# Kernel optimization log

Measured on AMD Instinct MI355X. Metric: run time of the kernel, lower is better.

## Reference

```python
import jax, jax.numpy as jnp
import numpy as np

NUM_CLUSTERS = 64
DIM = 512
ALPHA = 100.0
EPS = 1e-12  # torch F.normalize eps


def setup_inputs() -> dict:
    key = jax.random.key(0)
    k1, k2 = jax.random.split(key)
    x1 = jax.random.normal(k1, (30, DIM, 28, 28), dtype=jnp.float32)
    centroids = jax.random.uniform(k2, (NUM_CLUSTERS, DIM), dtype=jnp.float32)
    # _init_params: conv weight = 2*alpha*centroids (1x1 conv), bias = -alpha*||centroid||
    conv_w = 2.0 * ALPHA * centroids
    conv_b = -ALPHA * jnp.linalg.norm(centroids, axis=1)
    return {"x1": x1, "centroids": centroids, "conv_w": conv_w, "conv_b": conv_b}


def _l2norm(v, axis):
    n = jnp.sqrt(jnp.sum(v * v, axis=axis, keepdims=True))
    return v / jnp.maximum(n, EPS)


def reference(x1, centroids, conv_w, conv_b):
    T, C, H, W = x1.shape
    K, D = centroids.shape
    x = x1.reshape(T, C, H * W)            # [T, C, N]
    x = _l2norm(x, axis=1)                 # normalize_input: L2 over channel dim
    # 1x1 conv == matmul over channels: logits [T, K, N]
    logits = jnp.einsum('kc,tcn->tkn', conv_w, x) + conv_b[None, :, None]
    a = jax.nn.softmax(logits, axis=1)     # soft assignment over clusters
    # vlad[t,k,c] = sum_n a[t,k,n]*(x[t,c,n] - centroids[k,c])
    # rewritten as two small matmuls, avoiding the [K,C,N] residual tensor
    vlad = jnp.einsum('tkn,tcn->tkc', a, x) - a.sum(axis=-1)[:, :, None] * centroids[None]
    vlad = _l2norm(vlad, axis=2)           # intra-normalization over feature dim
    v = vlad.reshape(T, K * D)
    v = _l2norm(v, axis=1)                 # global L2 normalization
    return v.sum(axis=0, keepdims=True)    # [1, K*D] accumulated over 30 timesteps
```

## Files before the change

kernel.cpp:

```cpp
#include <hip/hip_runtime.h>
#include <math.h>

#define T_ 30
#define C_ 512
#define N_ 784
#define NA_ 800
#define XPITCH 520
#define EPSV 1e-12f

typedef __attribute__((ext_vector_type(8))) short bf16x8;
typedef __attribute__((ext_vector_type(4))) float f32x4;

__device__ __forceinline__ unsigned short f2bf(float f) {
    union { float f; unsigned int u; } v; v.f = f;
    unsigned int r = (v.u + 0x7FFFu + ((v.u >> 16) & 1u)) >> 16;
    return (unsigned short)r;
}
__device__ __forceinline__ float bf2f(unsigned short h) {
    union { unsigned int u; float f; } v; v.u = ((unsigned int)h) << 16;
    return v.f;
}

__global__ void k_prep(const float* __restrict__ w, unsigned short* __restrict__ wh,
                       unsigned short* __restrict__ wl) {
    int idx = blockIdx.x * 256 + threadIdx.x;
    float v = w[idx];
    unsigned short h = f2bf(v);
    wh[idx] = h;
    wl[idx] = f2bf(v - bf2f(h));
}

__global__ __launch_bounds__(256, 4) void k_assign(
    const float* __restrict__ x, const unsigned short* __restrict__ wh,
    const unsigned short* __restrict__ wl, const float* __restrict__ b,
    unsigned short* __restrict__ aT, float* __restrict__ asum)
{
    __shared__ __align__(16) char smem[2 * 16 * XPITCH * 2];
    unsigned short* xh = (unsigned short*)smem;
    unsigned short* xl = xh + 16 * XPITCH;
    float* red = (float*)smem;
    __shared__ float ssq[4][16];

    int t = blockIdx.y, n0 = blockIdx.x * 16;
    int tid = threadIdx.x;
    int w = tid >> 6, L = tid & 63, lid = L & 15, quad = L >> 4;
    int cbase = w * 128;
    int nseg = (L & 3) * 4;
    int crow = L >> 2;

    float4 q[8];
    #pragma unroll
    for (int p = 0; p < 8; ++p) {
        int c = cbase + p * 16 + crow;
        q[p] = *reinterpret_cast<const float4*>(
            x + ((size_t)t * C_ + c) * N_ + n0 + nseg);
    }
    float bk = b[L];

    const unsigned short* wha = wh + (size_t)lid * C_ + cbase + quad * 8;
    const unsigned short* wla = wl + (size_t)lid * C_ + cbase + quad * 8;
    bf16x8 cah[4], cal[4];
    #pragma unroll
    for (int mt = 0; mt < 4; ++mt) {
        cah[mt] = *reinterpret_cast<const bf16x8*>(wha + mt * 16 * C_);
        cal[mt] = *reinterpret_cast<const bf16x8*>(wla + mt * 16 * C_);
    }

    float ss0 = 0.f, ss1 = 0.f, ss2 = 0.f, ss3 = 0.f;
    #pragma unroll
    for (int p = 0; p < 8; ++p) {
        int c = cbase + p * 16 + crow;
        float vv[4] = {q[p].x, q[p].y, q[p].z, q[p].w};
        ss0 = fmaf(vv[0], vv[0], ss0); ss1 = fmaf(vv[1], vv[1], ss1);
        ss2 = fmaf(vv[2], vv[2], ss2); ss3 = fmaf(vv[3], vv[3], ss3);
        #pragma unroll
        for (int j = 0; j < 4; ++j) {
            unsigned short h = f2bf(vv[j]);
            xh[(nseg + j) * XPITCH + c] = h;
            xl[(nseg + j) * XPITCH + c] = f2bf(vv[j] - bf2f(h));
        }
    }
    #pragma unroll
    for (int m = 4; m <= 32; m <<= 1) {
        ss0 += __shfl_xor(ss0, m, 64); ss1 += __shfl_xor(ss1, m, 64);
        ss2 += __shfl_xor(ss2, m, 64); ss3 += __shfl_xor(ss3, m, 64);
    }
    if (L < 4) {
        ssq[w][L * 4 + 0] = ss0; ssq[w][L * 4 + 1] = ss1;
        ssq[w][L * 4 + 2] = ss2; ssq[w][L * 4 + 3] = ss3;
    }

    f32x4 acc[4];
    #pragma unroll
    for (int mt = 0; mt < 4; ++mt)
        #pragma unroll
        for (int r = 0; r < 4; ++r) acc[mt][r] = 0.f;

    #pragma unroll
    for (int ks = 0; ks < 4; ++ks) {
        bf16x8 nah[4], nal[4];
        #pragma unroll
        for (int mt = 0; mt < 4; ++mt) { nah[mt] = cah[mt]; nal[mt] = cal[mt]; }
        if (ks < 3) {
            #pragma unroll
            for (int mt = 0; mt < 4; ++mt) {
                nah[mt] = *reinterpret_cast<const bf16x8*>(
                    wha + mt * 16 * C_ + (ks + 1) * 32);
                nal[mt] = *reinterpret_cast<const bf16x8*>(
                    wla + mt * 16 * C_ + (ks + 1) * 32);
            }
        }
        int cs = cbase + ks * 32;
        bf16x8 bh = *reinterpret_cast<const bf16x8*>(&xh[lid * XPITCH + cs + quad * 8]);
        bf16x8 bl = *reinterpret_cast<const bf16x8*>(&xl[lid * XPITCH + cs + quad * 8]);
        #pragma unroll
        for (int mt = 0; mt < 4; ++mt) {
            acc[mt] = __builtin_amdgcn_mfma_f32_16x16x32_bf16(cah[mt], bh, acc[mt], 0, 0, 0);
            acc[mt] = __builtin_amdgcn_mfma_f32_16x16x32_bf16(cal[mt], bh, acc[mt], 0, 0, 0);
            acc[mt] = __builtin_amdgcn_mfma_f32_16x16x32_bf16(cah[mt], bl, acc[mt], 0, 0, 0);
        }
        #pragma unroll
        for (int mt = 0; mt < 4; ++mt) { cah[mt] = nah[mt]; cal[mt] = nal[mt]; }
    }
    __syncthreads();
    {
        float* rp = red + w * (16 * 68);
        #pragma unroll
        for (int mt = 0; mt < 4; ++mt)
            *reinterpret_cast<f32x4*>(&rp[lid * 68 + mt * 16 + quad * 4]) = acc[mt];
    }
    __syncthreads();

    float vv[4], iv[4];
    #pragma unroll
    for (int i = 0; i < 4; ++i) {
        int n = w * 4 + i;
        float s = ssq[0][n] + ssq[1][n] + ssq[2][n] + ssq[3][n];
        iv[i] = 1.0f / fmaxf(sqrtf(s), EPSV);
        float v = red[0 * 1088 + n * 68 + L] + red[1 * 1088 + n * 68 + L]
                + red[2 * 1088 + n * 68 + L] + red[3 * 1088 + n * 68 + L];
        vv[i] = fmaf(v, iv[i], bk);
    }
    float mx[4] = {vv[0], vv[1], vv[2], vv[3]};
    #pragma unroll
    for (int m = 1; m <= 32; m <<= 1) {
        #pragma unroll
        for (int i = 0; i < 4; ++i) mx[i] = fmaxf(mx[i], __shfl_xor(mx[i], m, 64));
    }
    float e[4], se[4];
    #pragma unroll
    for (int i = 0; i < 4; ++i) { e[i] = __expf(vv[i] - mx[i]); se[i] = e[i]; }
    #pragma unroll
    for (int m = 1; m <= 32; m <<= 1) {
        #pragma unroll
        for (int i = 0; i < 4; ++i) se[i] += __shfl_xor(se[i], m, 64);
    }
    float asl = 0.f;
    unsigned short av[4];
    #pragma unroll
    for (int i = 0; i < 4; ++i) {
        float a = e[i] / se[i];
        av[i] = f2bf(a * iv[i]);
        asl += a;
    }
    atomicAdd(&asum[t * 64 + L], asl);
    ushort4 st; st.x = av[0]; st.y = av[1]; st.z = av[2]; st.w = av[3];
    *reinterpret_cast<ushort4*>(aT + ((size_t)t * 64 + L) * NA_ + n0 + w * 4) = st;
    if (blockIdx.x == 48) {
        ushort4 z; z.x = 0; z.y = 0; z.z = 0; z.w = 0;
        *reinterpret_cast<ushort4*>(aT + ((size_t)t * 64 + L) * NA_ + 784 + w * 4) = z;
    }
}

__global__ __launch_bounds__(256) void k_vlad(
    const float* __restrict__ x, const unsigned short* __restrict__ aT,
    const float* __restrict__ asum, const float* __restrict__ cent,
    float* __restrict__ vlad, float* __restrict__ g2)
{
    __shared__ float red[4][16 * 68];
    int t = blockIdx.y, c0 = blockIdx.x * 16;
    int tid = threadIdx.x;
    int w = tid >> 6, L = tid & 63, lid = L & 15, quad = L >> 4;

    f32x4 acc[4];
    #pragma unroll
    for (int mt = 0; mt < 4; ++mt)
        #pragma unroll
        for (int r = 0; r < 4; ++r) acc[mt][r] = 0.f;

    const float* xrow = x + ((size_t)t * C_ + c0 + lid) * N_;
    const unsigned short* a0 = aT + (size_t)t * 64 * NA_ + (size_t)lid * NA_;

    int k = tid >> 2, cs4 = (tid & 3) * 4;
    float as = asum[t * 64 + k];
    float4 cv = *reinterpret_cast<const float4*>(cent + k * C_ + c0 + cs4);

    int nb = w * 32 + quad * 8;
    int nc = nb > 776 ? 776 : nb;
    float4 x0c = *reinterpret_cast<const float4*>(xrow + nc);
    float4 x1c = *reinterpret_cast<const float4*>(xrow + nc + 4);
    bf16x8 f0 = *reinterpret_cast<const bf16x8*>(a0 + nb);
    bf16x8 f1 = *reinterpret_cast<const bf16x8*>(a0 + 16 * NA_ + nb);
    bf16x8 f2 = *reinterpret_cast<const bf16x8*>(a0 + 32 * NA_ + nb);
    bf16x8 f3 = *reinterpret_cast<const bf16x8*>(a0 + 48 * NA_ + nb);

    for (int s = w; s < 25; s += 4) {
        int sn = s + 4;
        float4 x0n = x0c, x1n = x1c;
        bf16x8 g0 = f0, g1 = f1, g2v = f2, g3 = f3;
        if (sn < 25) {
            int nb2 = sn * 32 + quad * 8;
            int nc2 = nb2 > 776 ? 776 : nb2;
            x0n = *reinterpret_cast<const float4*>(xrow + nc2);
            x1n = *reinterpret_cast<const float4*>(xrow + nc2 + 4);
            g0 = *reinterpret_cast<const bf16x8*>(a0 + nb2);
            g1 = *reinterpret_cast<const bf16x8*>(a0 + 16 * NA_ + nb2);
            g2v = *reinterpret_cast<const bf16x8*>(a0 + 32 * NA_ + nb2);
            g3 = *reinterpret_cast<const bf16x8*>(a0 + 48 * NA_ + nb2);
        }
        bf16x8 bb;
        bb[0] = (short)f2bf(x0c.x); bb[1] = (short)f2bf(x0c.y);
        bb[2] = (short)f2bf(x0c.z); bb[3] = (short)f2bf(x0c.w);
        bb[4] = (short)f2bf(x1c.x); bb[5] = (short)f2bf(x1c.y);
        bb[6] = (short)f2bf(x1c.z); bb[7] = (short)f2bf(x1c.w);
        acc[0] = __builtin_amdgcn_mfma_f32_16x16x32_bf16(f0, bb, acc[0], 0, 0, 0);
        acc[1] = __builtin_amdgcn_mfma_f32_16x16x32_bf16(f1, bb, acc[1], 0, 0, 0);
        acc[2] = __builtin_amdgcn_mfma_f32_16x16x32_bf16(f2, bb, acc[2], 0, 0, 0);
        acc[3] = __builtin_amdgcn_mfma_f32_16x16x32_bf16(f3, bb, acc[3], 0, 0, 0);
        x0c = x0n; x1c = x1n; f0 = g0; f1 = g1; f2 = g2v; f3 = g3;
    }
    {
        float* rp = &red[w][0];
        #pragma unroll
        for (int mt = 0; mt < 4; ++mt)
            *reinterpret_cast<f32x4*>(&rp[lid * 68 + mt * 16 + quad * 4]) = acc[mt];
    }
    __syncthreads();

    float4 vout;
    float s2 = 0.f;
    #pragma unroll
    for (int j = 0; j < 4; ++j) {
        int cc = cs4 + j;
        float v = red[0][cc * 68 + k] + red[1][cc * 68 + k]
                + red[2][cc * 68 + k] + red[3][cc * 68 + k];
        v -= as * ((const float*)&cv)[j];
        ((float*)&vout)[j] = v;
        s2 = fmaf(v, v, s2);
    }
    *reinterpret_cast<float4*>(vlad + ((size_t)t * 64 + k) * C_ + c0 + cs4) = vout;
    s2 += __shfl_xor(s2, 1, 64);
    s2 += __shfl_xor(s2, 2, 64);
    if ((tid & 3) == 0) atomicAdd(&g2[t * 64 + k], s2);
}

__global__ __launch_bounds__(256) void k_out(
    const float* __restrict__ vlad, const float* __restrict__ g2,
    float* __restrict__ out)
{
    __shared__ float intr[1920];
    __shared__ float gl[1920];
    __shared__ float sinv[T_];
    int tid = threadIdx.x;
    for (int i = tid; i < 1920; i += 256) {
        float s = g2[i];
        gl[i] = s;
        intr[i] = 1.0f / fmaxf(sqrtf(s), EPSV);
    }
    __syncthreads();
    if (tid < T_) {
        float s = 0.f;
        #pragma unroll 8
        for (int k = 0; k < 64; ++k) {
            float iv = intr[tid * 64 + k];
            s += gl[tid * 64 + k] * iv * iv;
        }
        sinv[tid] = 1.0f / fmaxf(sqrtf(s), EPSV);
    }
    __syncthreads();
    int idx = blockIdx.x * 256 + tid;
    int k = idx >> 9;
    float s = 0.f;
    #pragma unroll 5
    for (int t = 0; t < T_; ++t)
        s += vlad[(size_t)t * 32768 + idx] * intr[t * 64 + k] * sinv[t];
    out[idx] = s;
}

extern "C" void kernel_launch(void* const* d_in, const int* in_sizes, int n_in,
                              void* d_out, int out_size, void* d_ws, size_t ws_size,
                              hipStream_t stream) {
    const float* x    = (const float*)d_in[0];
    const float* cent = (const float*)d_in[1];
    const float* w    = (const float*)d_in[2];
    const float* b    = (const float*)d_in[3];
    float* out = (float*)d_out;

    char* p = (char*)d_ws;
    unsigned short* wh = (unsigned short*)p;  p += 65536;
    unsigned short* wl = (unsigned short*)p;  p += 65536;
    float* asum = (float*)p;                  p += 1920 * 4;
    float* g2   = (float*)p;                  p += 1920 * 4;
    unsigned short* aT = (unsigned short*)p;  p += (size_t)T_ * 64 * NA_ * 2;
    float* vlad = (float*)p;                  p += (size_t)T_ * 64 * C_ * 4;

    k_prep<<<128, 256, 0, stream>>>(w, wh, wl);
    hipMemsetAsync(asum, 0, 2 * 1920 * 4, stream);
    k_assign<<<dim3(49, T_), 256, 0, stream>>>(x, wh, wl, b, aT, asum);
    k_vlad<<<dim3(32, T_), 256, 0, stream>>>(x, aT, asum, cent, vlad, g2);
    k_out<<<128, 256, 0, stream>>>(vlad, g2, out);
}
```

Baseline: 140.7 us.

## Split VLAD reduction over N halves, stream x through per-wave LDS, add g2 kernel

k_assign now stages x into per-wave LDS slices in two halves, shrinking shared memory so occupancy can rise to 8 blocks per SM, and it loads weights inline rather than prefetching them into registers. k_vlad splits the N dimension across two blocks per (c-tile, t) and accumulates into a zeroed vlad buffer with atomics. A new k_g2 kernel then computes the per-row squared norms, and k_out splits the T loop across two thread halves with twice as many blocks. This buys more parallelism at the cost of an extra memset of the vlad buffer, float atomics, and one more kernel launch.

Result: slower. 182.9 us (+30.0%).

```diff
diff --git a/kernel.cpp b/kernel.cpp
--- a/kernel.cpp
+++ b/kernel.cpp
@@ -5,7 +5,7 @@
 #define C_ 512
 #define N_ 784
 #define NA_ 800
-#define XPITCH 520
+#define SPITCH 72
 #define EPSV 1e-12f
 
 typedef __attribute__((ext_vector_type(8))) short bf16x8;
@@ -30,14 +30,14 @@
     wl[idx] = f2bf(v - bf2f(h));
 }
 
-__global__ __launch_bounds__(256, 4) void k_assign(
+__global__ __launch_bounds__(256, 8) void k_assign(
     const float* __restrict__ x, const unsigned short* __restrict__ wh,
     const unsigned short* __restrict__ wl, const float* __restrict__ b,
     unsigned short* __restrict__ aT, float* __restrict__ asum)
 {
-    __shared__ __align__(16) char smem[2 * 16 * XPITCH * 2];
+    __shared__ __align__(16) char smem[2 * 4 * 16 * SPITCH * 2];
     unsigned short* xh = (unsigned short*)smem;
-    unsigned short* xl = xh + 16 * XPITCH;
+    unsigned short* xl = xh + 4 * 16 * SPITCH;
     float* red = (float*)smem;
     __shared__ float ssq[4][16];
 
@@ -48,36 +48,57 @@
     int nseg = (L & 3) * 4;
     int crow = L >> 2;
 
-    float4 q[8];
-    #pragma unroll
-    for (int p = 0; p < 8; ++p) {
-        int c = cbase + p * 16 + crow;
-        q[p] = *reinterpret_cast<const float4*>(
-            x + ((size_t)t * C_ + c) * N_ + n0 + nseg);
-    }
-    float bk = b[L];
-
+    const float* xb = x + (size_t)t * C_ * N_ + n0 + nseg;
+    unsigned short* shh = xh + w * 16 * SPITCH;
+    unsigned short* shl = xl + w * 16 * SPITCH;
     const unsigned short* wha = wh + (size_t)lid * C_ + cbase + quad * 8;
     const unsigned short* wla = wl + (size_t)lid * C_ + cbase + quad * 8;
-    bf16x8 cah[4], cal[4];
-    #pragma unroll
-    for (int mt = 0; mt < 4; ++mt) {
-        cah[mt] = *reinterpret_cast<const bf16x8*>(wha + mt * 16 * C_);
-        cal[mt] = *reinterpret_cast<const bf16x8*>(wla + mt * 16 * C_);
-    }
-
+
+    float bk = b[L];
     float ss0 = 0.f, ss1 = 0.f, ss2 = 0.f, ss3 = 0.f;
-    #pragma unroll
-    for (int p = 0; p < 8; ++p) {
-        int c = cbase + p * 16 + crow;
-        float vv[4] = {q[p].x, q[p].y, q[p].z, q[p].w};
-        ss0 = fmaf(vv[0], vv[0], ss0); ss1 = fmaf(vv[1], vv[1], ss1);
-        ss2 = fmaf(vv[2], vv[2], ss2); ss3 = fmaf(vv[3], vv[3], ss3);
-        #pragma unroll
-        for (int j = 0; j < 4; ++j) {
-            unsigned short h = f2bf(vv[j]);
-            xh[(nseg + j) * XPITCH + c] = h;
-            xl[(nseg + j) * XPITCH + c] = f2bf(vv[j] - bf2f(h));
+    f32x4 acc[4];
+    #pragma unroll
+    for (int mt = 0; mt < 4; ++mt)
+        #pragma unroll
+        for (int r = 0; r < 4; ++r) acc[mt][r] = 0.f;
+
+    #pragma unroll
+    for (int half = 0; half < 2; ++half) {
+        float4 q[4];
+        #pragma unroll
+        for (int p = 0; p < 4; ++p)
+            q[p] = *reinterpret_cast<const float4*>(
+                xb + (size_t)(cbase + half * 64 + p * 16 + crow) * N_);
+        #pragma unroll
+        for (int p = 0; p < 4; ++p) {
+            int cl = p * 16 + crow;
+            float vv[4] = {q[p].x, q[p].y, q[p].z, q[p].w};
+            ss0 = fmaf(vv[0], vv[0], ss0); ss1 = fmaf(vv[1], vv[1], ss1);
+            ss2 = fmaf(vv[2], vv[2], ss2); ss3 = fmaf(vv[3], vv[3], ss3);
+            #pragma unroll
+            for (int j = 0; j < 4; ++j) {
+                unsigned short h = f2bf(vv[j]);
+                shh[(nseg + j) * SPITCH + cl] = h;
+                shl[(nseg + j) * SPITCH + cl] = f2bf(vv[j] - bf2f(h));
+            }
+        }
+        #pragma unroll
+        for (int ks2 = 0; ks2 < 2; ++ks2) {
+            bf16x8 bh = *reinterpret_cast<const bf16x8*>(
+                &shh[lid * SPITCH + ks2 * 32 + quad * 8]);
+            bf16x8 bl = *reinterpret_cast<const bf16x8*>(
+                &shl[lid * SPITCH + ks2 * 32 + quad * 8]);
+            int cg = half * 64 + ks2 * 32;
+            #pragma unroll
+            for (int mt = 0; mt < 4; ++mt) {
+                bf16x8 ah = *reinterpret_cast<const bf16x8*>(
+                    wha + (size_t)mt * 16 * C_ + cg);
+                bf16x8 al = *reinterpret_cast<const bf16x8*>(
+                    wla + (size_t)mt * 16 * C_ + cg);
+                acc[mt] = __builtin_amdgcn_mfma_f32_16x16x32_bf16(ah, bh, acc[mt], 0, 0, 0);
+                acc[mt] = __builtin_amdgcn_mfma_f32_16x16x32_bf16(al, bh, acc[mt], 0, 0, 0);
+                acc[mt] = __builtin_amdgcn_mfma_f32_16x16x32_bf16(ah, bl, acc[mt], 0, 0, 0);
+            }
         }
     }
     #pragma unroll
@@ -88,39 +109,6 @@
     if (L < 4) {
         ssq[w][L * 4 + 0] = ss0; ssq[w][L * 4 + 1] = ss1;
         ssq[w][L * 4 + 2] = ss2; ssq[w][L * 4 + 3] = ss3;
-    }
-
-    f32x4 acc[4];
-    #pragma unroll
-    for (int mt = 0; mt < 4; ++mt)
-        #pragma unroll
-        for (int r = 0; r < 4; ++r) acc[mt][r] = 0.f;
-
-    #pragma unroll
-    for (int ks = 0; ks < 4; ++ks) {
-        bf16x8 nah[4], nal[4];
-        #pragma unroll
-        for (int mt = 0; mt < 4; ++mt) { nah[mt] = cah[mt]; nal[mt] = cal[mt]; }
-        if (ks < 3) {
-            #pragma unroll
-            for (int mt = 0; mt < 4; ++mt) {
-                nah[mt] = *reinterpret_cast<const bf16x8*>(
-                    wha + mt * 16 * C_ + (ks + 1) * 32);
-                nal[mt] = *reinterpret_cast<const bf16x8*>(
-                    wla + mt * 16 * C_ + (ks + 1) * 32);
-            }
-        }
-        int cs = cbase + ks * 32;
-        bf16x8 bh = *reinterpret_cast<const bf16x8*>(&xh[lid * XPITCH + cs + quad * 8]);
-        bf16x8 bl = *reinterpret_cast<const bf16x8*>(&xl[lid * XPITCH + cs + quad * 8]);
-        #pragma unroll
-        for (int mt = 0; mt < 4; ++mt) {
-            acc[mt] = __builtin_amdgcn_mfma_f32_16x16x32_bf16(cah[mt], bh, acc[mt], 0, 0, 0);
-            acc[mt] = __builtin_amdgcn_mfma_f32_16x16x32_bf16(cal[mt], bh, acc[mt], 0, 0, 0);
-            acc[mt] = __builtin_amdgcn_mfma_f32_16x16x32_bf16(cah[mt], bl, acc[mt], 0, 0, 0);
-        }
-        #pragma unroll
-        for (int mt = 0; mt < 4; ++mt) { cah[mt] = nah[mt]; cal[mt] = nal[mt]; }
     }
     __syncthreads();
     {
@@ -172,13 +160,13 @@
     }
 }
 
-__global__ __launch_bounds__(256) void k_vlad(
+__global__ __launch_bounds__(256, 6) void k_vlad(
     const float* __restrict__ x, const unsigned short* __restrict__ aT,
     const float* __restrict__ asum, const float* __restrict__ cent,
-    float* __restrict__ vlad, float* __restrict__ g2)
+    float* __restrict__ vlad)
 {
     __shared__ float red[4][16 * 68];
-    int t = blockIdx.y, c0 = blockIdx.x * 16;
+    int t = blockIdx.z, nh = blockIdx.y, c0 = blockIdx.x * 16;
     int tid = threadIdx.x;
     int w = tid >> 6, L = tid & 63, lid = L & 15, quad = L >> 4;
 
@@ -192,10 +180,13 @@
     const unsigned short* a0 = aT + (size_t)t * 64 * NA_ + (size_t)lid * NA_;
 
     int k = tid >> 2, cs4 = (tid & 3) * 4;
-    float as = asum[t * 64 + k];
+    float as = nh ? 0.f : asum[t * 64 + k];
     float4 cv = *reinterpret_cast<const float4*>(cent + k * C_ + c0 + cs4);
 
-    int nb = w * 32 + quad * 8;
+    int send = nh ? 25 : 13;
+    int s0 = nh * 13 + w;
+
+    int nb = s0 * 32 + quad * 8;
     int nc = nb > 776 ? 776 : nb;
     float4 x0c = *reinterpret_cast<const float4*>(xrow + nc);
     float4 x1c = *reinterpret_cast<const float4*>(xrow + nc + 4);
@@ -204,11 +195,11 @@
     bf16x8 f2 = *reinterpret_cast<const bf16x8*>(a0 + 32 * NA_ + nb);
     bf16x8 f3 = *reinterpret_cast<const bf16x8*>(a0 + 48 * NA_ + nb);
 
-    for (int s = w; s < 25; s += 4) {
+    for (int s = s0; s < send; s += 4) {
         int sn = s + 4;
         float4 x0n = x0c, x1n = x1c;
         bf16x8 g0 = f0, g1 = f1, g2v = f2, g3 = f3;
-        if (sn < 25) {
+        if (sn < send) {
             int nb2 = sn * 32 + quad * 8;
             int nc2 = nb2 > 776 ? 776 : nb2;
             x0n = *reinterpret_cast<const float4*>(xrow + nc2);
@@ -237,21 +228,32 @@
     }
     __syncthreads();
 
-    float4 vout;
-    float s2 = 0.f;
+    float* dst = vlad + ((size_t)t * 64 + k) * C_ + c0 + cs4;
     #pragma unroll
     for (int j = 0; j < 4; ++j) {
         int cc = cs4 + j;
         float v = red[0][cc * 68 + k] + red[1][cc * 68 + k]
                 + red[2][cc * 68 + k] + red[3][cc * 68 + k];
         v -= as * ((const float*)&cv)[j];
-        ((float*)&vout)[j] = v;
-        s2 = fmaf(v, v, s2);
-    }
-    *reinterpret_cast<float4*>(vlad + ((size_t)t * 64 + k) * C_ + c0 + cs4) = vout;
-    s2 += __shfl_xor(s2, 1, 64);
-    s2 += __shfl_xor(s2, 2, 64);
-    if ((tid & 3) == 0) atomicAdd(&g2[t * 64 + k], s2);
+        atomicAdd(dst + j, v);
+    }
+}
+
+__global__ __launch_bounds__(256) void k_g2(const float* __restrict__ vlad,
+                                            float* __restrict__ g2) {
+    int tid = threadIdx.x;
+    int w = tid >> 6, L = tid & 63;
+    int r = blockIdx.x * 4 + w;
+    const float* p = vlad + (size_t)r * C_;
+    float s = 0.f;
+    #pragma unroll
+    for (int i = 0; i < 2; ++i) {
+        float4 a = *reinterpret_cast<const float4*>(p + i * 256 + L * 4);
+        s = fmaf(a.x, a.x, fmaf(a.y, a.y, fmaf(a.z, a.z, fmaf(a.w, a.w, s))));
+    }
+    #pragma unroll
+    for (int m = 1; m <= 32; m <<= 1) s += __shfl_xor(s, m, 64);
+    if (L == 0) g2[r] = s;
 }
 
 __global__ __launch_bounds__(256) void k_out(
@@ -261,6 +263,7 @@
     __shared__ float intr[1920];
     __shared__ float gl[1920];
     __shared__ float sinv[T_];
+    __shared__ float part[256];
     int tid = threadIdx.x;
     for (int i = tid; i < 1920; i += 256) {
         float s = g2[i];
@@ -278,13 +281,16 @@
         sinv[tid] = 1.0f / fmaxf(sqrtf(s), EPSV);
     }
     __syncthreads();
-    int idx = blockIdx.x * 256 + tid;
+    int idx = blockIdx.x * 128 + (tid & 127);
+    int th = tid >> 7;
     int k = idx >> 9;
     float s = 0.f;
-    #pragma unroll 5
-    for (int t = 0; t < T_; ++t)
+    #pragma unroll
+    for (int t = th * 15; t < th * 15 + 15; ++t)
         s += vlad[(size_t)t * 32768 + idx] * intr[t * 64 + k] * sinv[t];
-    out[idx] = s;
+    part[tid] = s;
+    __syncthreads();
+    if (tid < 128) out[idx] = part[tid] + part[tid + 128];
 }
 
 extern "C" void kernel_launch(void* const* d_in, const int* in_sizes, int n_in,
@@ -300,13 +306,14 @@
     unsigned short* wh = (unsigned short*)p;  p += 65536;
     unsigned short* wl = (unsigned short*)p;  p += 65536;
     float* asum = (float*)p;                  p += 1920 * 4;
+    float* vlad = (float*)p;                  p += (size_t)T_ * 64 * C_ * 4;
     float* g2   = (float*)p;                  p += 1920 * 4;
     unsigned short* aT = (unsigned short*)p;  p += (size_t)T_ * 64 * NA_ * 2;
-    float* vlad = (float*)p;                  p += (size_t)T_ * 64 * C_ * 4;
 
     k_prep<<<128, 256, 0, stream>>>(w, wh, wl);
-    hipMemsetAsync(asum, 0, 2 * 1920 * 4, stream);
+    hipMemsetAsync(asum, 0, 1920 * 4 + (size_t)T_ * 64 * C_ * 4, stream);
     k_assign<<<dim3(49, T_), 256, 0, stream>>>(x, wh, wl, b, aT, asum);
-    k_vlad<<<dim3(32, T_), 256, 0, stream>>>(x, aT, asum, cent, vlad, g2);
-    k_out<<<128, 256, 0, stream>>>(vlad, g2, out);
-}
+    k_vlad<<<dim3(32, 2, T_), 256, 0, stream>>>(x, aT, asum, cent, vlad);
+    k_g2<<<480, 256, 0, stream>>>(vlad, g2);
+    k_out<<<256, 256, 0, stream>>>(vlad, g2, out);
+}
```
